# Optimization experiments

Measured on AMD Instinct MI355X. Metric: run time of the kernel, lower is better.

The kernel has to match this reference:

```python
import jax, jax.numpy as jnp
import numpy as np

H = 300  # hidden size hardcoded in the module
VX = 32000
VY = 32000
NX, NY, B = 128, 128, 256


def setup_inputs() -> dict:
    key = jax.random.key(0)
    ks = jax.random.split(key, 10)
    s = 1.0 / np.sqrt(H)
    x = jax.random.randint(ks[0], (NX, B), 0, VX)
    y = jax.random.randint(ks[1], (NY, B), 0, VY)
    # padding_idx=0: zero the pad row of each embedding table
    enc_emb = jax.random.normal(ks[2], (VX, H), jnp.float32).at[0].set(0.0)
    encW = jax.random.uniform(ks[3], (H, H), jnp.float32, -s, s)
    encb = jax.random.uniform(ks[4], (H,), jnp.float32, -s, s)
    dec_emb = jax.random.normal(ks[5], (VY, H), jnp.float32).at[0].set(0.0)
    decW = jax.random.uniform(ks[6], (H, H), jnp.float32, -s, s)
    decb = jax.random.uniform(ks[7], (H,), jnp.float32, -s, s)
    outW = jax.random.uniform(ks[8], (VY, H), jnp.float32, -s, s)
    outb = jax.random.uniform(ks[9], (VY,), jnp.float32, -s, s)
    return {"x": x, "y": y, "enc_emb": enc_emb, "encW": encW, "encb": encb,
            "dec_emb": dec_emb, "decW": decW, "decb": decb,
            "outW": outW, "outb": outb}


def reference(x, y, enc_emb, encW, encb, dec_emb, decW, decb, outW, outb):
    # Encoder: Elman recurrence h = relu(e_x[i] + W h + b)
    e_x = enc_emb[x]                                  # [NX, B, H]
    h0 = jnp.zeros((x.shape[1], H), e_x.dtype)        # h=0 broadcast over batch

    def enc_step(h, ex):
        return jax.nn.relu(ex + h @ encW.T + encb), None

    h, _ = jax.lax.scan(enc_step, h0, e_x)

    # Decoder: teacher-forced recurrence with per-step mean cross-entropy
    e_y = dec_emb[y]                                  # [NY, B, H]

    def dec_step(h, inp):
        ey, tgt = inp
        h = jax.nn.relu(ey + h @ decW.T + decb)
        logits = h @ outW.T + outb                    # [B, VY]
        logp = jax.nn.log_softmax(logits, axis=-1)
        ce = -jnp.mean(jnp.take_along_axis(logp, tgt[:, None], axis=-1))
        return h, ce

    _, ces = jax.lax.scan(dec_step, h, (e_y[:-1], y[1:]))
    return jnp.sum(ces)
```

## Files before the change

kernel.cpp:

```cpp
#include <hip/hip_runtime.h>
#include <hip/hip_bf16.h>
#include <stdint.h>

typedef unsigned short u16;
typedef unsigned char u8;
typedef float f32x4 __attribute__((ext_vector_type(4)));
typedef float f32x2 __attribute__((ext_vector_type(2)));
typedef _Float16 f16x2 __attribute__((ext_vector_type(2)));
typedef _Float16 f16x8 __attribute__((ext_vector_type(8)));

#define H      300
#define KP     320
#define BATCH  256
#define NX     128
#define NY     128
#define VY     32000
#define NPAD   32768
#define MROWS  32512


#define OWS_OFF   0UL
#define OWS_BYTES ((unsigned long)NPAD * KP)
#define OWS_PAD   131072UL
#define A8_OFF    (OWS_OFF + OWS_BYTES + OWS_PAD)
#define A8_BYTES  ((unsigned long)MROWS * KP)
#define WTE_OFF   (A8_OFF + A8_BYTES)
#define WT_BYTES  (320UL * KP * 4)
#define WTD_OFF   (WTE_OFF + WT_BYTES)
#define OBP_OFF   (WTD_OFF + WT_BYTES)
#define OBP_BYTES ((unsigned long)NPAD * 4)
#define SE_OFF    (OBP_OFF + OBP_BYTES)
#define SE_BYTES  ((unsigned long)MROWS * 4)

__global__ __launch_bounds__(256) void k0_prep(const float* __restrict__ outW,
                                               const float* __restrict__ encW,
                                               const float* __restrict__ decW,
                                               const float* __restrict__ outb,
                                               u8* __restrict__ ows,
                                               float* __restrict__ obp,
                                               float* __restrict__ wte,
                                               float* __restrict__ wtd) {
    long id = (long)blockIdx.x * 256 + threadIdx.x;
    const long n1 = (long)NPAD * KP / 4;
    if (id < n1) {
        int v = (int)(id / 80), k4 = (int)(id % 80) * 4;
        float4 f = {0.f, 0.f, 0.f, 0.f};
        if (v < VY && k4 < H) f = *(const float4*)&outW[(long)v * H + k4];
        int w = __builtin_amdgcn_cvt_pk_fp8_f32(f.x, f.y, 0, false);
        w = __builtin_amdgcn_cvt_pk_fp8_f32(f.z, f.w, w, true);
        long dst = (long)(v >> 6) * 20480 + (k4 >> 5) * 2048 + ((v >> 4) & 3) * 512
                 + (v & 15) * 8 + ((k4 >> 3) & 3) * 128 + (k4 & 7);
        *(unsigned int*)(ows + dst) = (unsigned int)w;
        return;
    }
    long id2 = id - n1;
    if (id2 < NPAD) {
        obp[id2] = (id2 < VY) ? outb[id2] : -1e30f;
        return;
    }
    id2 -= NPAD;
    if (id2 < 320L * KP) {
        int k = (int)(id2 / KP), j = (int)(id2 % KP);
        wte[id2] = (k < H && j < H) ? encW[j * H + k] : 0.f;
        return;
    }
    id2 -= 320L * KP;
    if (id2 < 320L * KP) {
        int k = (int)(id2 / KP), j = (int)(id2 % KP);
        wtd[id2] = (k < H && j < H) ? decW[j * H + k] : 0.f;
    }
}

__global__ __launch_bounds__(640) void k1_rnn(const int* __restrict__ x,
                                              const int* __restrict__ y,
                                              const float* __restrict__ enc_emb,
                                              const float* __restrict__ dec_emb,
                                              const float* __restrict__ encb,
                                              const float* __restrict__ decb,
                                              const float* __restrict__ wte,
                                              const float* __restrict__ wtd,
                                              u8* __restrict__ A8) {
    const int tid = threadIdx.x;
    const int s = tid / 160;
    const int j = tid - s * 160;
    const int b = blockIdx.x;

    __shared__ __align__(16) _Float16 hh[320];
    __shared__ float part[1280];
    __shared__ __align__(4) u8 a8row[320];

    for (int i = tid; i < 320; i += 640) hh[i] = (_Float16)0.f;

    const bool comb = (tid < 320);
    const int jc = tid;
    const float be = (comb && jc < H) ? encb[jc] : 0.f;
    const float bd = (comb && jc < H) ? decb[jc] : 0.f;

    f16x2 wa[40], wc[40];
#pragma unroll
    for (int kk = 0; kk < 40; ++kk) {
        int k0 = s * 80 + 2 * kk;
        wa[kk] = (f16x2){(_Float16)wte[k0 * KP + j],       (_Float16)wte[(k0 + 1) * KP + j]};
        wc[kk] = (f16x2){(_Float16)wte[k0 * KP + j + 160], (_Float16)wte[(k0 + 1) * KP + j + 160]};
    }

    int idx_n = x[BATCH + b];
    float e_cur = 0.f;
    if (comb && jc < H) e_cur = enc_emb[(long)x[b] * H + jc];
    __syncthreads();

    const f16x8* hb8 = (const f16x8*)&hh[s * 80];

    for (int t = 0; t < NX; ++t) {
        int idx_n2 = x[min(t + 2, NX - 1) * BATCH + b];
        float e_nx = 0.f;
        if (comb && jc < H && t + 1 < NX) e_nx = enc_emb[(long)idx_n * H + jc];

        float p0 = 0.f, p1 = 0.f;
#pragma unroll
        for (int i = 0; i < 10; ++i) {
            f16x8 hv = hb8[i];
            f16x2 q0 = {hv[0], hv[1]}, q1 = {hv[2], hv[3]};
            f16x2 q2 = {hv[4], hv[5]}, q3 = {hv[6], hv[7]};
            p0 = __builtin_amdgcn_fdot2(wa[4 * i + 0], q0, p0, false);
            p1 = __builtin_amdgcn_fdot2(wc[4 * i + 0], q0, p1, false);
            p0 = __builtin_amdgcn_fdot2(wa[4 * i + 1], q1, p0, false);
            p1 = __builtin_amdgcn_fdot2(wc[4 * i + 1], q1, p1, false);
            p0 = __builtin_amdgcn_fdot2(wa[4 * i + 2], q2, p0, false);
            p1 = __builtin_amdgcn_fdot2(wc[4 * i + 2], q2, p1, false);
            p0 = __builtin_amdgcn_fdot2(wa[4 * i + 3], q3, p0, false);
            p1 = __builtin_amdgcn_fdot2(wc[4 * i + 3], q3, p1, false);
        }
        part[s * 320 + j] = p0;
        part[s * 320 + 160 + j] = p1;
        __syncthreads();
        if (comb) {
            float v = part[jc] + part[320 + jc] + part[640 + jc] + part[960 + jc] + be + e_cur;
            hh[jc] = (_Float16)fmaxf(v, 0.f);
        }
        __syncthreads();
        e_cur = e_nx; idx_n = idx_n2;
    }

#pragma unroll
    for (int kk = 0; kk < 40; ++kk) {
        int k0 = s * 80 + 2 * kk;
        wa[kk] = (f16x2){(_Float16)wtd[k0 * KP + j],       (_Float16)wtd[(k0 + 1) * KP + j]};
        wc[kk] = (f16x2){(_Float16)wtd[k0 * KP + j + 160], (_Float16)wtd[(k0 + 1) * KP + j + 160]};
    }

    idx_n = y[BATCH + b];
    e_cur = 0.f;
    if (comb && jc < H) e_cur = dec_emb[(long)y[b] * H + jc];

    for (int t = 0; t < NY - 1; ++t) {
        int idx_n2 = y[min(t + 2, NY - 1) * BATCH + b];
        float e_nx = 0.f;
        if (comb && jc < H && t + 1 < NY - 1) e_nx = dec_emb[(long)idx_n * H + jc];

        float p0 = 0.f, p1 = 0.f;
#pragma unroll
        for (int i = 0; i < 10; ++i) {
            f16x8 hv = hb8[i];
            f16x2 q0 = {hv[0], hv[1]}, q1 = {hv[2], hv[3]};
            f16x2 q2 = {hv[4], hv[5]}, q3 = {hv[6], hv[7]};
            p0 = __builtin_amdgcn_fdot2(wa[4 * i + 0], q0, p0, false);
            p1 = __builtin_amdgcn_fdot2(wc[4 * i + 0], q0, p1, false);
            p0 = __builtin_amdgcn_fdot2(wa[4 * i + 1], q1, p0, false);
            p1 = __builtin_amdgcn_fdot2(wc[4 * i + 1], q1, p1, false);
            p0 = __builtin_amdgcn_fdot2(wa[4 * i + 2], q2, p0, false);
            p1 = __builtin_amdgcn_fdot2(wc[4 * i + 2], q2, p1, false);
            p0 = __builtin_amdgcn_fdot2(wa[4 * i + 3], q3, p0, false);
            p1 = __builtin_amdgcn_fdot2(wc[4 * i + 3], q3, p1, false);
        }
        part[s * 320 + j] = p0;
        part[s * 320 + 160 + j] = p1;
        __syncthreads();
        if (comb) {
            float v = part[jc] + part[320 + jc] + part[640 + jc] + part[960 + jc] + bd + e_cur;
            v = fmaxf(v, 0.f);
            hh[jc] = (_Float16)v;
            int pk = __builtin_amdgcn_cvt_pk_fp8_f32(v, v, 0, false);
            a8row[jc] = (u8)(pk & 0xff);
        }
        __syncthreads();
        if (tid < 80)
            ((unsigned int*)(A8 + (long)(t * BATCH + b) * KP))[tid] =
                ((const unsigned int*)a8row)[tid];
        e_cur = e_nx; idx_n = idx_n2;
    }
}

__global__ __launch_bounds__(256, 2) void k2_gemm(const u8* __restrict__ A8,
                                                  const u8* __restrict__ OWS,
                                                  const float* __restrict__ obp,
                                                  float* __restrict__ sumexp) {
    const int tid = threadIdx.x;
    const int lane = tid & 63, wave = tid >> 6;
    const int lane16 = lane & 15, quad = lane >> 4;
    const int cg = blockIdx.x & 7;
    const int rb = blockIdx.x >> 3;
    const int colbase = cg * 4096;

    __shared__ float rowsum[64];
    if (tid < 64) rowsum[tid] = 0.f;
    __syncthreads();

    long a[4][10];
    {
        const u8* abase = A8 + ((long)rb * 64 + lane16) * KP + quad * 8;
#pragma unroll
        for (int rt = 0; rt < 4; ++rt)
#pragma unroll
            for (int ks = 0; ks < 10; ++ks)
                a[rt][ks] = *(const long*)(abase + rt * 16 * KP + ks * 32);
    }

    const u8* wb = OWS + (long)(cg * 64 + wave) * 20480 + lane * 8;

    float rsum[16];
#pragma unroll
    for (int i = 0; i < 16; ++i) rsum[i] = 0.f;

    long nb0[4], nb1[4];
#pragma unroll
    for (int tc = 0; tc < 4; ++tc) {
        nb0[tc] = *(const long*)(wb + tc * 512);
        nb1[tc] = *(const long*)(wb + 2048 + tc * 512);
    }

    for (int ct = 0; ct < 16; ++ct) {
        const u8* ctp = wb + (long)ct * 81920;
        f32x4 acc[4][4];
#pragma unroll
        for (int p = 0; p < 4; ++p)
#pragma unroll
            for (int q = 0; q < 4; ++q) acc[p][q] = (f32x4){0.f, 0.f, 0.f, 0.f};

#pragma unroll
        for (int rt = 0; rt < 4; ++rt)
#pragma unroll
            for (int tc = 0; tc < 4; ++tc)
                acc[rt][tc] = __builtin_amdgcn_mfma_f32_16x16x32_fp8_fp8(
                    a[rt][0], nb0[tc], acc[rt][tc], 0, 0, 0);
#pragma unroll
        for (int rt = 0; rt < 4; ++rt)
#pragma unroll
            for (int tc = 0; tc < 4; ++tc)
                acc[rt][tc] = __builtin_amdgcn_mfma_f32_16x16x32_fp8_fp8(
                    a[rt][1], nb1[tc], acc[rt][tc], 0, 0, 0);

#pragma unroll
        for (int ks = 2; ks < 10; ++ks) {
            const u8* p = ctp + ks * 2048;
            long bfr[4];
#pragma unroll
            for (int tc = 0; tc < 4; ++tc)
                bfr[tc] = *(const long*)(p + tc * 512);
#pragma unroll
            for (int rt = 0; rt < 4; ++rt)
#pragma unroll
                for (int tc = 0; tc < 4; ++tc)
                    acc[rt][tc] = __builtin_amdgcn_mfma_f32_16x16x32_fp8_fp8(
                        a[rt][ks], bfr[tc], acc[rt][tc], 0, 0, 0);
        }

        {
            const u8* np = wb + (long)min(ct + 1, 15) * 81920;
#pragma unroll
            for (int tc = 0; tc < 4; ++tc) {
                nb0[tc] = *(const long*)(np + tc * 512);
                nb1[tc] = *(const long*)(np + 2048 + tc * 512);
            }
        }

        int cb = colbase + ct * 256 + wave * 64;
#pragma unroll
        for (int tc = 0; tc < 4; ++tc) {
            float ob = obp[cb + tc * 16 + lane16];
#pragma unroll
            for (int rt = 0; rt < 4; ++rt)
#pragma unroll
                for (int i = 0; i < 4; ++i)
                    rsum[rt * 4 + i] += __expf(acc[rt][tc][i] + ob);
        }
    }

#pragma unroll
    for (int m = 1; m < 16; m <<= 1)
#pragma unroll
        for (int i = 0; i < 16; ++i) rsum[i] += __shfl_xor(rsum[i], m, 64);
    if (lane16 == 0) {
#pragma unroll
        for (int rt = 0; rt < 4; ++rt)
#pragma unroll
            for (int i = 0; i < 4; ++i)
                atomicAdd(&rowsum[rt * 16 + quad * 4 + i], rsum[rt * 4 + i]);
    }
    __syncthreads();
    if (tid < 64) atomicAdd(&sumexp[(long)rb * 64 + tid], rowsum[tid]);
}

__global__ __launch_bounds__(256) void k3_ce(const u8* __restrict__ A8,
                                             const u8* __restrict__ OWS,
                                             const float* __restrict__ outb,
                                             const float* __restrict__ sumexp,
                                             const int* __restrict__ y,
                                             float* __restrict__ out) {
    const int wave = threadIdx.x >> 6, lane = threadIdx.x & 63;
    const int r = blockIdx.x * 4 + wave;
    const int t = r >> 8, b = r & 255;
    const int tgt = y[(t + 1) * BATCH + b];
    float s = 0.f;
    if (lane < 40) {
        unsigned long long av = *(const unsigned long long*)(A8 + (long)r * KP + lane * 8);
        long wdst = (long)(tgt >> 6) * 20480 + (lane >> 2) * 2048
                  + ((tgt >> 4) & 3) * 512 + (tgt & 15) * 8 + (lane & 3) * 128;
        unsigned long long wv = *(const unsigned long long*)(OWS + wdst);
        unsigned int a4 = (unsigned int)av, a4h = (unsigned int)(av >> 32);
        unsigned int w4 = (unsigned int)wv, w4h = (unsigned int)(wv >> 32);
        f32x2 al = __builtin_amdgcn_cvt_pk_f32_fp8(a4, false);
        f32x2 ah = __builtin_amdgcn_cvt_pk_f32_fp8(a4, true);
        f32x2 wl = __builtin_amdgcn_cvt_pk_f32_fp8(w4, false);
        f32x2 wh = __builtin_amdgcn_cvt_pk_f32_fp8(w4, true);
        s += al[0] * wl[0] + al[1] * wl[1] + ah[0] * wh[0] + ah[1] * wh[1];
        al = __builtin_amdgcn_cvt_pk_f32_fp8(a4h, false);
        ah = __builtin_amdgcn_cvt_pk_f32_fp8(a4h, true);
        wl = __builtin_amdgcn_cvt_pk_f32_fp8(w4h, false);
        wh = __builtin_amdgcn_cvt_pk_f32_fp8(w4h, true);
        s += al[0] * wl[0] + al[1] * wl[1] + ah[0] * wh[0] + ah[1] * wh[1];
    }
#pragma unroll
    for (int m = 1; m < 64; m <<= 1) s += __shfl_xor(s, m, 64);
    __shared__ float part[4];
    if (lane == 0) part[wave] = logf(sumexp[r]) - (s + outb[tgt]);
    __syncthreads();
    if (threadIdx.x == 0) {
        float tot = part[0] + part[1] + part[2] + part[3];
        atomicAdd(out, tot * (1.0f / 256.0f));
    }
}

extern "C" void kernel_launch(void* const* d_in, const int* in_sizes, int n_in,
                              void* d_out, int out_size, void* d_ws, size_t ws_size,
                              hipStream_t stream) {
    (void)in_sizes; (void)n_in; (void)out_size; (void)ws_size;
    const int*   x       = (const int*)d_in[0];
    const int*   y       = (const int*)d_in[1];
    const float* enc_emb = (const float*)d_in[2];
    const float* encW    = (const float*)d_in[3];
    const float* encb    = (const float*)d_in[4];
    const float* dec_emb = (const float*)d_in[5];
    const float* decW    = (const float*)d_in[6];
    const float* decb    = (const float*)d_in[7];
    const float* outW    = (const float*)d_in[8];
    const float* outb    = (const float*)d_in[9];

    char* ws = (char*)d_ws;
    u8* ows  = (u8*)(ws + OWS_OFF);
    u8* A8   = (u8*)(ws + A8_OFF);
    float* wte    = (float*)(ws + WTE_OFF);
    float* wtd    = (float*)(ws + WTD_OFF);
    float* obp    = (float*)(ws + OBP_OFF);
    float* sumexp = (float*)(ws + SE_OFF);

    hipMemsetAsync(sumexp, 0, SE_BYTES, stream);
    hipMemsetAsync(d_out, 0, sizeof(float), stream);

    long n0 = (long)NPAD * KP / 4 + NPAD + 2L * 320 * KP;
    k0_prep<<<(int)((n0 + 255) / 256), 256, 0, stream>>>(outW, encW, decW, outb,
                                                         ows, obp, wte, wtd);
    k1_rnn<<<256, 640, 0, stream>>>(x, y, enc_emb, dec_emb, encb, decb, wte, wtd, A8);
    k2_gemm<<<508 * 8, 256, 0, stream>>>(A8, ows, obp, sumexp);
    k3_ce<<<8128, 256, 0, stream>>>(A8, ows, outb, sumexp, y, (float*)d_out);
}
```

Baseline: 1.010 ms.

## Stage weight tiles in LDS via async copies shared across waves in GEMM

The logits GEMM is restructured so each block covers 256 rows, with every wave owning 64 rows, over a 1024-column slice. Weight tiles are double-buffered in shared memory through global_load_lds async copies, so all four waves reuse the same B tile instead of each streaming its own from global memory. The bias exponential is precomputed once, turning exp(x+b) into exp(x)*exp(b), and the per-block shared-memory reduction is replaced by direct global atomics. This adds a barrier per column tile and changes padded columns to use exp(b)=0, which keeps them out of the sum.

```diff
diff --git a/kernel.cpp b/kernel.cpp
--- a/kernel.cpp
+++ b/kernel.cpp
@@ -32,12 +32,17 @@
 #define SE_OFF    (OBP_OFF + OBP_BYTES)
 #define SE_BYTES  ((unsigned long)MROWS * 4)
 
+#define ASYNC_COPY16(dst_lds, src_glb)                                          \
+    __builtin_amdgcn_global_load_lds(                                           \
+        (const __attribute__((address_space(1))) unsigned int*)(src_glb),       \
+        (__attribute__((address_space(3))) unsigned int*)(dst_lds), 16, 0, 0)
+
 __global__ __launch_bounds__(256) void k0_prep(const float* __restrict__ outW,
                                                const float* __restrict__ encW,
                                                const float* __restrict__ decW,
                                                const float* __restrict__ outb,
                                                u8* __restrict__ ows,
-                                               float* __restrict__ obp,
+                                               float* __restrict__ eob,
                                                float* __restrict__ wte,
                                                float* __restrict__ wtd) {
     long id = (long)blockIdx.x * 256 + threadIdx.x;
@@ -55,7 +60,7 @@
     }
     long id2 = id - n1;
     if (id2 < NPAD) {
-        obp[id2] = (id2 < VY) ? outb[id2] : -1e30f;
+        eob[id2] = (id2 < VY) ? __expf(outb[id2]) : 0.f;
         return;
     }
     id2 -= NPAD;
@@ -193,22 +198,23 @@
 
 __global__ __launch_bounds__(256, 2) void k2_gemm(const u8* __restrict__ A8,
                                                   const u8* __restrict__ OWS,
-                                                  const float* __restrict__ obp,
+                                                  const float* __restrict__ eob,
                                                   float* __restrict__ sumexp) {
     const int tid = threadIdx.x;
     const int lane = tid & 63, wave = tid >> 6;
     const int lane16 = lane & 15, quad = lane >> 4;
-    const int cg = blockIdx.x & 7;
-    const int rb = blockIdx.x >> 3;
-    const int colbase = cg * 4096;
-
-    __shared__ float rowsum[64];
-    if (tid < 64) rowsum[tid] = 0.f;
-    __syncthreads();
+    const int bid = blockIdx.x;
+    const int cg8 = bid & 7;
+    const int cs  = (bid >> 3) & 3;
+    const int rb  = bid >> 5;
+    const int colbase = cg8 * 4096 + cs * 1024;
+    const long tile0 = (long)(colbase >> 6);
+
+    __shared__ __align__(16) u8 bt[2][20480];
 
     long a[4][10];
     {
-        const u8* abase = A8 + ((long)rb * 64 + lane16) * KP + quad * 8;
+        const u8* abase = A8 + ((long)rb * 256 + wave * 64 + lane16) * KP + quad * 8;
 #pragma unroll
         for (int rt = 0; rt < 4; ++rt)
 #pragma unroll
@@ -216,21 +222,30 @@
                 a[rt][ks] = *(const long*)(abase + rt * 16 * KP + ks * 32);
     }
 
-    const u8* wb = OWS + (long)(cg * 64 + wave) * 20480 + lane * 8;
+    {
+        const u8* src = OWS + tile0 * 20480 + (wave << 10) + (lane << 4);
+        u8* dst = &bt[0][wave << 10];
+#pragma unroll
+        for (int r = 0; r < 5; ++r)
+            ASYNC_COPY16(dst + r * 4096, src + r * 4096);
+    }
+    __syncthreads();
 
     float rsum[16];
 #pragma unroll
     for (int i = 0; i < 16; ++i) rsum[i] = 0.f;
 
-    long nb0[4], nb1[4];
-#pragma unroll
-    for (int tc = 0; tc < 4; ++tc) {
-        nb0[tc] = *(const long*)(wb + tc * 512);
-        nb1[tc] = *(const long*)(wb + 2048 + tc * 512);
-    }
-
     for (int ct = 0; ct < 16; ++ct) {
-        const u8* ctp = wb + (long)ct * 81920;
+        const u8* bb = &bt[ct & 1][0];
+
+        if (ct < 15) {
+            const u8* src = OWS + (tile0 + ct + 1) * 20480 + (wave << 10) + (lane << 4);
+            u8* dst = &bt[(ct + 1) & 1][wave << 10];
+#pragma unroll
+            for (int r = 0; r < 5; ++r)
+                ASYNC_COPY16(dst + r * 4096, src + r * 4096);
+        }
+
         f32x4 acc[4][4];
 #pragma unroll
         for (int p = 0; p < 4; ++p)
@@ -238,25 +253,11 @@
             for (int q = 0; q < 4; ++q) acc[p][q] = (f32x4){0.f, 0.f, 0.f, 0.f};
 
 #pragma unroll
-        for (int rt = 0; rt < 4; ++rt)
+        for (int ks = 0; ks < 10; ++ks) {
+            long bfr[4];
 #pragma unroll
             for (int tc = 0; tc < 4; ++tc)
-                acc[rt][tc] = __builtin_amdgcn_mfma_f32_16x16x32_fp8_fp8(
-                    a[rt][0], nb0[tc], acc[rt][tc], 0, 0, 0);
-#pragma unroll
-        for (int rt = 0; rt < 4; ++rt)
-#pragma unroll
-            for (int tc = 0; tc < 4; ++tc)
-                acc[rt][tc] = __builtin_amdgcn_mfma_f32_16x16x32_fp8_fp8(
-                    a[rt][1], nb1[tc], acc[rt][tc], 0, 0, 0);
-
-#pragma unroll
-        for (int ks = 2; ks < 10; ++ks) {
-            const u8* p = ctp + ks * 2048;
-            long bfr[4];
-#pragma unroll
-            for (int tc = 0; tc < 4; ++tc)
-                bfr[tc] = *(const long*)(p + tc * 512);
+                bfr[tc] = *(const long*)(bb + ks * 2048 + tc * 512 + lane * 8);
 #pragma unroll
             for (int rt = 0; rt < 4; ++rt)
 #pragma unroll
@@ -265,25 +266,18 @@
                         a[rt][ks], bfr[tc], acc[rt][tc], 0, 0, 0);
         }
 
-        {
-            const u8* np = wb + (long)min(ct + 1, 15) * 81920;
-#pragma unroll
-            for (int tc = 0; tc < 4; ++tc) {
-                nb0[tc] = *(const long*)(np + tc * 512);
-                nb1[tc] = *(const long*)(np + 2048 + tc * 512);
-            }
-        }
-
-        int cb = colbase + ct * 256 + wave * 64;
+        int cb = colbase + ct * 64;
 #pragma unroll
         for (int tc = 0; tc < 4; ++tc) {
-            float ob = obp[cb + tc * 16 + lane16];
+            float eb = eob[cb + tc * 16 + lane16];
 #pragma unroll
             for (int rt = 0; rt < 4; ++rt)
 #pragma unroll
                 for (int i = 0; i < 4; ++i)
-                    rsum[rt * 4 + i] += __expf(acc[rt][tc][i] + ob);
-        }
+                    rsum[rt * 4 + i] += __expf(acc[rt][tc][i]) * eb;
+        }
+
+        __syncthreads();
     }
 
 #pragma unroll
@@ -291,14 +285,13 @@
 #pragma unroll
         for (int i = 0; i < 16; ++i) rsum[i] += __shfl_xor(rsum[i], m, 64);
     if (lane16 == 0) {
+        float* sp = &sumexp[(long)rb * 256 + wave * 64];
 #pragma unroll
         for (int rt = 0; rt < 4; ++rt)
 #pragma unroll
             for (int i = 0; i < 4; ++i)
-                atomicAdd(&rowsum[rt * 16 + quad * 4 + i], rsum[rt * 4 + i]);
-    }
-    __syncthreads();
-    if (tid < 64) atomicAdd(&sumexp[(long)rb * 64 + tid], rowsum[tid]);
+                atomicAdd(&sp[rt * 16 + quad * 4 + i], rsum[rt * 4 + i]);
+    }
 }
 
 __global__ __launch_bounds__(256) void k3_ce(const u8* __restrict__ A8,
@@ -361,7 +354,7 @@
     u8* A8   = (u8*)(ws + A8_OFF);
     float* wte    = (float*)(ws + WTE_OFF);
     float* wtd    = (float*)(ws + WTD_OFF);
-    float* obp    = (float*)(ws + OBP_OFF);
+    float* eob    = (float*)(ws + OBP_OFF);
     float* sumexp = (float*)(ws + SE_OFF);
 
     hipMemsetAsync(sumexp, 0, SE_BYTES, stream);
@@ -369,8 +362,8 @@
 
     long n0 = (long)NPAD * KP / 4 + NPAD + 2L * 320 * KP;
     k0_prep<<<(int)((n0 + 255) / 256), 256, 0, stream>>>(outW, encW, decW, outb,
-                                                         ows, obp, wte, wtd);
+                                                         ows, eob, wte, wtd);
     k1_rnn<<<256, 640, 0, stream>>>(x, y, enc_emb, dec_emb, encb, decb, wte, wtd, A8);
-    k2_gemm<<<508 * 8, 256, 0, stream>>>(A8, ows, obp, sumexp);
+    k2_gemm<<<127 * 32, 256, 0, stream>>>(A8, ows, eob, sumexp);
     k3_ce<<<8128, 256, 0, stream>>>(A8, ows, outb, sumexp, y, (float*)d_out);
 }
```

Result: faster. 962.7 us (-4.7%).
